# Optimization experiments

Hardware: AMD Instinct MI355X
Metric: run time of the kernel (lower is better)

Reference implementation:

```python
import jax, jax.numpy as jnp
import numpy as np

B, S, H, V, C = 32, 512, 256, 50000, 5
NUM_LAYERS, WINDOW = 2, 2


def setup_inputs() -> dict:
    key = jax.random.key(0)
    ks = jax.random.split(key, 24)
    std = 0.1  # matches nn.init.normal_(p, 0, 0.1)
    n = lambda k, shp: jax.random.normal(k, shp, dtype=jnp.float32) * std
    u = lambda k, shp: -0.05 + jax.random.uniform(k, shp, dtype=jnp.float32) * 0.1
    return {
        "input_sentences": jax.random.randint(ks[0], (B, S), 0, V),
        "sentences_length": jax.random.randint(ks[1], (B,), 1, S),
        "hh0": u(ks[2], (B, S, H)),
        "cs0": u(ks[3], (B, S, H)),
        "embed": n(ks[4], (V, H)),
        # stacked word-gate weights, gate order: i, l, r, f, s, output, u
        "W_lr": n(ks[5], (7, H, 2 * H)),
        "W_c": n(ks[6], (7, H, H)),
        "W_x": n(ks[7], (7, H, H)),
        "W_g": n(ks[8], (7, H, H)),
        "gate_bias": n(ks[9], (7, H)),
        # sentence-state gates
        "W_fg_g": n(ks[10], (H, H)),
        "W_fg_h": n(ks[11], (H, H)),
        "W_fgi_g": n(ks[12], (H, H)),
        "W_fgi_h": n(ks[13], (H, H)),
        "W_og_g": n(ks[14], (H, H)),
        "W_og_h": n(ks[15], (H, H)),
        "b_fg": n(ks[16], (H,)),
        "b_fgi": n(ks[17], (H,)),
        # output head
        "W1": n(ks[18], (H, 2 * H)),
        "b1": n(ks[19], (H,)),
        "Wout": n(ks[20], (C, H)),
        "bout": n(ks[21], (C,)),
    }


def _before_sum(x, window):
    # sum of right-shifted (zero-padded at front) copies, shifts 1..window
    out = jnp.zeros_like(x)
    for s in range(1, window + 1):
        out = out + jnp.pad(x[:, :-s], ((0, 0), (s, 0), (0, 0)))
    return out


def _after_sum(x, window):
    out = jnp.zeros_like(x)
    for s in range(1, window + 1):
        out = out + jnp.pad(x[:, s:], ((0, 0), (0, s), (0, 0)))
    return out


def _slstm_step(hh, cs, sv, scs, wv, W_lr, W_c, W_x, W_g, gate_bias,
                W_fg_g, W_fg_h, W_fgi_g, W_fgi_h, W_og_g, W_og_h, b_fg, b_fgi):
    avg_hh = hh.mean(axis=1)                                   # [B,H]
    f_hat_g = jax.nn.sigmoid(sv @ W_fg_g.T + avg_hh @ W_fg_h.T + b_fg)
    # NOTE: original code (faithfully) uses output_gate_bias here, not output_gate_g_bias
    og_g = jax.nn.sigmoid(sv @ W_og_g.T + avg_hh @ W_og_h.T + gate_bias[5])
    f_hat_g_i = jax.nn.sigmoid((sv @ W_fgi_g.T)[:, None] + hh @ W_fgi_h.T + b_fgi)
    scores = jax.nn.softmax(f_hat_g_i, axis=2)                 # over hidden dim
    new_scs = jax.nn.softmax(f_hat_g, axis=1) * scs + (scores * cs).sum(axis=1)
    new_sv = og_g * jnp.tanh(new_scs)

    hb = _before_sum(hh, WINDOW)
    ha = _after_sum(hh, WINDOW)
    cb = _before_sum(cs, WINDOW)
    ca = _after_sum(cs, WINDOW)
    ba = jnp.concatenate([hb, ha], axis=-1)                    # [B,S,2H]

    # all 7 gate pre-activations at once: [B,S,7,H]
    pre = (jnp.einsum('bsk,ghk->bsgh', ba, W_lr)
           + jnp.einsum('bsk,ghk->bsgh', hh, W_c)
           + jnp.einsum('bsk,ghk->bsgh', wv, W_x)
           + (jnp.einsum('bk,ghk->bgh', new_sv, W_g) + gate_bias)[:, None])

    g5 = jax.nn.sigmoid(pre[..., :5, :])                       # i,l,r,f,s
    b_, s_ = g5.shape[:2]
    # joint softmax over the concatenated 5*H gate vector (as in torch cat+softmax)
    g5 = jax.nn.softmax(g5.reshape(b_, s_, -1), axis=-1).reshape(b_, s_, 5, -1)
    i_t, l_t, r_t, f_t, s_t = (g5[..., k, :] for k in range(5))
    og = jax.nn.sigmoid(pre[..., 5, :])
    u_g = jnp.tanh(pre[..., 6, :])

    new_cs = l_t * cb + f_t * cs + r_t * ca + s_t * scs[:, None] + i_t * u_g
    new_hh = og * jnp.tanh(new_cs)
    return new_hh, new_cs, new_sv, new_scs


def reference(input_sentences, sentences_length, hh0, cs0, embed,
              W_lr, W_c, W_x, W_g, gate_bias,
              W_fg_g, W_fg_h, W_fgi_g, W_fgi_h, W_og_g, W_og_h, b_fg, b_fgi,
              W1, b1, Wout, bout):
    wv = embed[input_sentences]                                # [B,S,H]
    hh, cs = hh0, cs0
    sv, scs = hh0.mean(axis=1), cs0.mean(axis=1)
    for _ in range(NUM_LAYERS):
        hh, cs, sv, scs = _slstm_step(hh, cs, sv, scs, wv,
                                      W_lr, W_c, W_x, W_g, gate_bias,
                                      W_fg_g, W_fg_h, W_fgi_g, W_fgi_h,
                                      W_og_g, W_og_h, b_fg, b_fgi)
    avg_hh = hh.mean(axis=1)
    conc = jnp.concatenate([avg_hh, sv], axis=1) @ W1.T + b1
    fc = conc @ Wout.T + bout
    return jax.nn.log_softmax(fc, axis=1), sv
```

## Files before the change

kernel.cpp:

```cpp
#include <hip/hip_runtime.h>
#include <stdint.h>
#include <math.h>

#define B_   32
#define S_   512
#define H_   256
#define M_   (B_*S_)
#define KBIG 1024
#define NB   1792
#define C_   5

typedef __bf16 bf16;
typedef __bf16 bf16x8 __attribute__((ext_vector_type(8)));
typedef float  floatx4 __attribute__((ext_vector_type(4)));

__device__ __forceinline__ float sigm(float x){ return 1.f/(1.f+expf(-x)); }

__device__ __forceinline__ void gl16(const bf16* g, bf16* l){
    __builtin_amdgcn_global_load_lds(
        (const __attribute__((address_space(1))) unsigned int*)g,
        (__attribute__((address_space(3))) unsigned int*)l, 16, 0, 0);
}

__global__ void wcomb_k(const float* __restrict__ Wlr, const float* __restrict__ Wc,
                        const float* __restrict__ Wx, bf16* __restrict__ WT){
    int n = blockIdx.x;
    int g = n >> 8, h = n & 255;
    int k4 = threadIdx.x * 4;
    const float* src;
    if (k4 < 512)      src = Wlr + ((size_t)(g*256 + h))*512 + k4;
    else if (k4 < 768) src = Wc  + ((size_t)(g*256 + h))*256 + (k4 - 512);
    else               src = Wx  + ((size_t)(g*256 + h))*256 + (k4 - 768);
    float4 v = *(const float4*)src;
    bf16 o[4] = {(bf16)v.x,(bf16)v.y,(bf16)v.z,(bf16)v.w};
    *(uint2*)&WT[(size_t)n*KBIG + k4] = *(uint2*)o;
}

__global__ void cvtw_k(const float* __restrict__ a, bf16* __restrict__ o){
    int i4 = (blockIdx.x*256 + threadIdx.x)*4;
    float4 v = *(const float4*)(a + i4);
    bf16 t[4] = {(bf16)v.x,(bf16)v.y,(bf16)v.z,(bf16)v.w};
    *(uint2*)(o + i4) = *(uint2*)t;
}

__global__ void gather_k(const int* __restrict__ idx, const float* __restrict__ embed,
                         bf16* __restrict__ wv){
    int i4 = (blockIdx.x*256 + threadIdx.x)*4;
    int m = i4 >> 8, h = i4 & 255;
    float4 v = *(const float4*)(embed + (size_t)idx[m]*H_ + h);
    bf16 o[4] = {(bf16)v.x,(bf16)v.y,(bf16)v.z,(bf16)v.w};
    *(uint2*)(wv + (size_t)m*H_ + h) = *(uint2*)o;
}

__global__ void mean1_k(const float* __restrict__ x, float* __restrict__ part){
    int b = blockIdx.x, c = blockIdx.y, h = threadIdx.x;
    const float* p = x + ((size_t)b*S_ + c*32)*H_ + h;
    float s = 0.f;
    #pragma unroll 8
    for (int t=0;t<32;t++) s += p[(size_t)t*H_];
    part[((size_t)b*16 + c)*H_ + h] = s;
}
__global__ void mean2_k(const float* __restrict__ part, float* __restrict__ out){
    int b = blockIdx.x, h = threadIdx.x;
    float s = 0.f;
    #pragma unroll
    for (int c=0;c<16;c++) s += part[((size_t)b*16 + c)*H_ + h];
    out[b*H_ + h] = s * (1.f/512.f);
}

__global__ void buildx_k(const float* __restrict__ hh, const bf16* __restrict__ wv,
                         bf16* __restrict__ X){
    int m = blockIdx.x, h = threadIdx.x;
    int s = m & (S_-1);
    size_t base = (size_t)m*H_ + h;
    float hb = (s>=1    ? hh[base - H_] : 0.f) + (s>=2    ? hh[base - 2*H_] : 0.f);
    float ha = (s<=S_-2 ? hh[base + H_] : 0.f) + (s<=S_-3 ? hh[base + 2*H_] : 0.f);
    bf16* xr = X + (size_t)m*KBIG;
    xr[h]     = (bf16)hb;
    xr[256+h] = (bf16)ha;
    xr[512+h] = (bf16)hh[base];
    xr[768+h] = wv[base];
}

__global__ void mv5_k(const float* __restrict__ sv, const float* __restrict__ avg,
    const float* __restrict__ Wfg_g, const float* __restrict__ Wfg_h,
    const float* __restrict__ Wog_g, const float* __restrict__ Wog_h,
    const float* __restrict__ Wfgi_g, float* __restrict__ res){
    int j = blockIdx.x, b = blockIdx.y, h = threadIdx.x;
    const float* vec = (j==1 || j==3) ? avg + b*H_ : sv + b*H_;
    const float* W   = (j==0)?Wfg_g:(j==1)?Wfg_h:(j==2)?Wog_g:(j==3)?Wog_h:Wfgi_g;
    __shared__ float v[H_];
    v[h] = vec[h]; __syncthreads();
    const float* w = W + (size_t)h*H_;
    float d = 0.f;
    for (int k=0;k<H_;k++) d += v[k]*w[k];
    res[((size_t)b*5 + j)*H_ + h] = d;
}
__global__ void comb_k(const float* __restrict__ res, const float* __restrict__ b_fg,
                       const float* __restrict__ gbias, const float* __restrict__ b_fgi,
                       float* __restrict__ fhg, float* __restrict__ ogg,
                       float* __restrict__ svg){
    int b = blockIdx.x, h = threadIdx.x;
    const float* r = res + (size_t)b*5*H_;
    fhg[b*H_+h] = sigm(r[h] + r[H_+h] + b_fg[h]);
    ogg[b*H_+h] = sigm(r[2*H_+h] + r[3*H_+h] + gbias[5*H_+h]);
    svg[b*H_+h] = r[4*H_+h] + b_fgi[h];
}

template<int EPI>
__global__ __launch_bounds__(256)
void mgemm_k(const bf16* __restrict__ A, const bf16* __restrict__ BT,
             bf16* __restrict__ C, const float* __restrict__ gt,
             int Kdim, int lda, int ldb, int ldc){
    __shared__ alignas(16) bf16 lsA[128*32];
    __shared__ alignas(16) bf16 lsB[128*32];
    int tid  = threadIdx.x;
    int m0 = blockIdx.y * 128, n0 = blockIdx.x * 128;
    int wave = tid >> 6, lane = tid & 63;
    int wm = (wave & 1) * 64, wn = (wave >> 1) * 64;
    int lrow = lane & 15, quad = lane >> 4;

    floatx4 zero = {0.f,0.f,0.f,0.f};
    floatx4 acc[4][4];
    #pragma unroll
    for (int i=0;i<4;i++)
        #pragma unroll
        for (int j=0;j<4;j++) acc[i][j] = zero;

    int srow = tid >> 2;
    int scol = (tid & 3) * 8;
    const bf16* Abase = A  + (size_t)(m0 + srow)*lda + scol;
    const bf16* Bbase = BT + (size_t)(n0 + srow)*ldb + scol;
    bf16* dA0 = &lsA[srow*32 + scol];
    bf16* dA1 = &lsA[(64+srow)*32 + scol];
    bf16* dB0 = &lsB[srow*32 + scol];
    bf16* dB1 = &lsB[(64+srow)*32 + scol];

    for (int k0 = 0; k0 < Kdim; k0 += 32){
        __syncthreads();
        gl16(Abase + k0,                     dA0);
        gl16(Abase + (size_t)64*lda + k0,    dA1);
        gl16(Bbase + k0,                     dB0);
        gl16(Bbase + (size_t)64*ldb + k0,    dB1);
        __syncthreads();
        bf16x8 af[4], bfr[4];
        #pragma unroll
        for (int mi=0;mi<4;mi++) af[mi]  = *(const bf16x8*)&lsA[(wm+mi*16+lrow)*32 + quad*8];
        #pragma unroll
        for (int ni=0;ni<4;ni++) bfr[ni] = *(const bf16x8*)&lsB[(wn+ni*16+lrow)*32 + quad*8];
        #pragma unroll
        for (int mi=0;mi<4;mi++)
            #pragma unroll
            for (int ni=0;ni<4;ni++)
                acc[mi][ni] = __builtin_amdgcn_mfma_f32_16x16x32_bf16(af[mi], bfr[ni], acc[mi][ni], 0, 0, 0);
    }

    #pragma unroll
    for (int mi=0;mi<4;mi++)
        #pragma unroll
        for (int ni=0;ni<4;ni++){
            int row = m0 + wm + mi*16 + quad*4;
            int col = n0 + wn + ni*16 + lrow;
            #pragma unroll
            for (int r=0;r<4;r++){
                float v = acc[mi][ni][r];
                if (EPI) v += gt[(size_t)((row+r)>>9)*NB + col];
                C[(size_t)(row+r)*ldc + col] = (bf16)v;
            }
        }
}

__global__ void scorep_k(const bf16* __restrict__ fgih, const float* __restrict__ svg,
                         const float* __restrict__ cs, float* __restrict__ part){
    int chunk = blockIdx.x, b = blockIdx.y;
    int tid = threadIdx.x, wave = tid >> 6, lane = tid & 63;
    __shared__ float acc4[4][256];
    float sw[4], acc[4] = {0.f,0.f,0.f,0.f};
    #pragma unroll
    for (int j=0;j<4;j++) sw[j] = svg[b*H_ + lane + 64*j];
    for (int t=wave; t<16; t+=4){
        int m = b*S_ + chunk*16 + t;
        const bf16* fr = fgih + (size_t)m*H_;
        float e[4], loc = 0.f;
        #pragma unroll
        for (int j=0;j<4;j++){ e[j] = expf(sigm(sw[j] + (float)fr[lane+64*j])); loc += e[j]; }
        #pragma unroll
        for (int off=32; off; off>>=1) loc += __shfl_xor(loc, off, 64);
        float inv = 1.f/loc;
        const float* cr = cs + (size_t)m*H_;
        #pragma unroll
        for (int j=0;j<4;j++) acc[j] += e[j]*inv*cr[lane+64*j];
    }
    #pragma unroll
    for (int j=0;j<4;j++) acc4[wave][lane+64*j] = acc[j];
    __syncthreads();
    part[((size_t)b*32 + chunk)*H_ + tid] =
        acc4[0][tid] + acc4[1][tid] + acc4[2][tid] + acc4[3][tid];
}

__global__ void newscs_k(const float* __restrict__ part, const float* __restrict__ fhg,
                         const float* __restrict__ ogg, const float* __restrict__ scs_in,
                         float* __restrict__ scs_out, float* __restrict__ sv_out){
    int b = blockIdx.x, h = threadIdx.x;
    __shared__ float r[256];
    float dot = 0.f;
    #pragma unroll 8
    for (int c=0;c<32;c++) dot += part[((size_t)b*32+c)*H_ + h];
    float e = expf(fhg[b*H_+h]);
    r[h] = e; __syncthreads();
    for (int off=128; off; off>>=1){ if (h<off) r[h] += r[h+off]; __syncthreads(); }
    float ns = (e / r[0]) * scs_in[b*H_+h] + dot;
    scs_out[b*H_+h] = ns;
    sv_out[b*H_+h]  = ogg[b*H_+h] * tanhf(ns);
}

__global__ void gterm_k(const float* __restrict__ svn, const float* __restrict__ Wg,
                        const float* __restrict__ gbias, float* __restrict__ gt){
    int g = blockIdx.x, b = blockIdx.y, h = threadIdx.x;
    __shared__ float s[H_];
    s[h] = svn[b*H_+h]; __syncthreads();
    const float* w = Wg + ((size_t)g*H_ + h)*H_;
    float d = 0.f;
    for (int k=0;k<H_;k++) d += s[k]*w[k];
    gt[(size_t)b*NB + g*H_ + h] = d + gbias[g*H_+h];
}

__global__ void gates_k(const bf16* __restrict__ pre, const float* __restrict__ cs_in,
                        const float* __restrict__ scs_in,
                        float* __restrict__ hh_out, float* __restrict__ cs_out){
    int tid = threadIdx.x, wave = tid >> 6, lane = tid & 63;
    int m = blockIdx.x*4 + wave;
    int b = m >> 9, s = m & (S_-1);
    const bf16* row = pre + (size_t)m*NB;
    float ex[4][5], og[4], u[4];
    float loc = 0.f;
    #pragma unroll
    for (int j=0;j<4;j++){
        int h = lane + 64*j;
        #pragma unroll
        for (int g=0; g<5; ++g){
            float e = expf(sigm((float)row[g*H_ + h]));
            ex[j][g] = e; loc += e;
        }
        og[j] = sigm((float)row[5*H_ + h]);
        u[j]  = tanhf((float)row[6*H_ + h]);
    }
    #pragma unroll
    for (int off=32; off; off>>=1) loc += __shfl_xor(loc, off, 64);
    float inv = 1.f / loc;
    #pragma unroll
    for (int j=0;j<4;j++){
        int h = lane + 64*j;
        size_t i = (size_t)m*H_ + h;
        float cb = (s>=1    ? cs_in[i - H_] : 0.f) + (s>=2    ? cs_in[i - 2*H_] : 0.f);
        float ca = (s<=S_-2 ? cs_in[i + H_] : 0.f) + (s<=S_-3 ? cs_in[i + 2*H_] : 0.f);
        float nc = ex[j][1]*inv*cb + ex[j][3]*inv*cs_in[i] + ex[j][2]*inv*ca
                 + ex[j][4]*inv*scs_in[b*H_+h] + ex[j][0]*inv*u[j];
        cs_out[i] = nc;
        hh_out[i] = og[j] * tanhf(nc);
    }
}

__global__ void head_k(const float* __restrict__ avgh, const float* __restrict__ sv,
                       const float* __restrict__ W1, const float* __restrict__ b1,
                       const float* __restrict__ Wout, const float* __restrict__ bout,
                       float* __restrict__ out){
    int b = blockIdx.x, t = threadIdx.x;
    __shared__ float conc[H_];
    __shared__ float fc[8];
    const float* wr = W1 + (size_t)t*512;
    float d = b1[t];
    for (int k=0;k<H_;k++) d += avgh[b*H_+k]*wr[k];
    for (int k=0;k<H_;k++) d += sv[b*H_+k]*wr[256+k];
    conc[t] = d;
    __syncthreads();
    if (t < C_){
        const float* wo = Wout + (size_t)t*H_;
        float s = bout[t];
        for (int i=0;i<H_;i++) s += conc[i]*wo[i];
        fc[t] = s;
    }
    __syncthreads();
    if (t == 0){
        float mx = fc[0];
        for (int c=1;c<C_;c++) mx = fmaxf(mx, fc[c]);
        float se = 0.f;
        for (int c=0;c<C_;c++) se += expf(fc[c]-mx);
        float lse = mx + logf(se);
        for (int c=0;c<C_;c++) out[b*C_+c] = fc[c]-lse;
    }
    out[B_*C_ + b*H_ + t] = sv[b*H_+t];
}

extern "C" void kernel_launch(void* const* d_in, const int* in_sizes, int n_in,
                              void* d_out, int out_size, void* d_ws, size_t ws_size,
                              hipStream_t stream){
    const int*   idx    = (const int*)d_in[0];
    const float* hh0    = (const float*)d_in[2];
    const float* cs0    = (const float*)d_in[3];
    const float* embed  = (const float*)d_in[4];
    const float* Wlr    = (const float*)d_in[5];
    const float* Wc     = (const float*)d_in[6];
    const float* Wx     = (const float*)d_in[7];
    const float* Wg     = (const float*)d_in[8];
    const float* gbias  = (const float*)d_in[9];
    const float* Wfg_g  = (const float*)d_in[10];
    const float* Wfg_h  = (const float*)d_in[11];
    const float* Wfgi_g = (const float*)d_in[12];
    const float* Wfgi_h = (const float*)d_in[13];
    const float* Wog_g  = (const float*)d_in[14];
    const float* Wog_h  = (const float*)d_in[15];
    const float* b_fg   = (const float*)d_in[16];
    const float* b_fgi  = (const float*)d_in[17];
    const float* W1     = (const float*)d_in[18];
    const float* b1     = (const float*)d_in[19];
    const float* Wout   = (const float*)d_in[20];
    const float* bout   = (const float*)d_in[21];

    uint8_t* p = (uint8_t*)d_ws;
    auto alloc = [&](size_t bytes)->void*{ void* r=(void*)p; p += (bytes + 255) & ~(size_t)255; return r; };
    bf16*  WT    = (bf16*)alloc((size_t)NB*KBIG*2);
    bf16*  WfgiT = (bf16*)alloc((size_t)H_*H_*2);
    bf16*  X     = (bf16*)alloc((size_t)M_*KBIG*2);
    bf16*  wv    = (bf16*)alloc((size_t)M_*H_*2);
    bf16*  pre   = (bf16*)alloc((size_t)M_*NB*2);
    bf16*  fgih  = (bf16*)alloc((size_t)M_*H_*2);
    float* hhA = (float*)alloc((size_t)M_*H_*4);
    float* csA = (float*)alloc((size_t)M_*H_*4);
    float* hhB = (float*)alloc((size_t)M_*H_*4);
    float* csB = (float*)alloc((size_t)M_*H_*4);
    float* mpart= (float*)alloc((size_t)B_*16*H_*4);
    float* part = (float*)alloc((size_t)B_*32*H_*4);
    float* res5 = (float*)alloc((size_t)B_*5*H_*4);
    float* avgh = (float*)alloc(B_*H_*4);
    float* fhg  = (float*)alloc(B_*H_*4);
    float* ogg  = (float*)alloc(B_*H_*4);
    float* svg  = (float*)alloc(B_*H_*4);
    float* svP0 = (float*)alloc(B_*H_*4);
    float* svP1 = (float*)alloc(B_*H_*4);
    float* scP0 = (float*)alloc(B_*H_*4);
    float* scP1 = (float*)alloc(B_*H_*4);
    float* gt   = (float*)alloc((size_t)B_*NB*4);

    wcomb_k <<<NB,          256, 0, stream>>>(Wlr, Wc, Wx, WT);
    cvtw_k  <<<(H_*H_)/1024,256, 0, stream>>>(Wfgi_h, WfgiT);
    gather_k<<<(M_*H_)/1024,256, 0, stream>>>(idx, embed, wv);
    mean1_k <<<dim3(B_,16), 256, 0, stream>>>(hh0, mpart);
    mean2_k <<<B_,          256, 0, stream>>>(mpart, svP0);
    mean1_k <<<dim3(B_,16), 256, 0, stream>>>(cs0, mpart);
    mean2_k <<<B_,          256, 0, stream>>>(mpart, scP0);

    const float *hin = hh0, *cin = cs0;
    float *hout = hhA, *cout = csA;
    float *svin = svP0, *scin = scP0, *svout = svP1, *scout = scP1;

    for (int l=0; l<2; ++l){
        const float* avgp;
        if (l == 0){
            avgp = svin;
        } else {
            mean1_k<<<dim3(B_,16), 256, 0, stream>>>(hin, mpart);
            mean2_k<<<B_,          256, 0, stream>>>(mpart, avgh);
            avgp = avgh;
        }
        mv5_k   <<<dim3(5,B_), 256, 0, stream>>>(svin, avgp, Wfg_g, Wfg_h, Wog_g,
                                                 Wog_h, Wfgi_g, res5);
        comb_k  <<<B_, 256, 0, stream>>>(res5, b_fg, gbias, b_fgi, fhg, ogg, svg);
        buildx_k<<<M_, 256, 0, stream>>>(hin, wv, X);
        mgemm_k<0><<<dim3(2,128), 256, 0, stream>>>(X+512, WfgiT, fgih, nullptr,
                                                    H_, KBIG, H_, H_);
        scorep_k<<<dim3(32,B_), 256, 0, stream>>>(fgih, svg, cin, part);
        newscs_k<<<B_, 256, 0, stream>>>(part, fhg, ogg, scin, scout, svout);
        gterm_k <<<dim3(7,B_), 256, 0, stream>>>(svout, Wg, gbias, gt);
        mgemm_k<1><<<dim3(14,128), 256, 0, stream>>>(X, WT, pre, gt,
                                                     KBIG, KBIG, KBIG, NB);
        gates_k <<<M_/4, 256, 0, stream>>>(pre, cin, scin, hout, cout);
        hin = hout; cin = cout;
        hout = (l==0) ? hhB : hhA;
        cout = (l==0) ? csB : csA;
        float* q;
        q = svin; svin = svout; svout = q;
        q = scin; scin = scout; scout = q;
    }
    mean1_k<<<dim3(B_,16), 256, 0, stream>>>(hin, mpart);
    mean2_k<<<B_,          256, 0, stream>>>(mpart, avgh);
    head_k <<<B_, 256, 0, stream>>>(avgh, svin, W1, b1, Wout, bout, (float*)d_out);
}
```

Measured before the change: 571.8 us.

## Widen GEMM tiles to 128x256 and vectorize elementwise kernels with float4 loads

The bf16 MFMA GEMM now computes a 128x256 output tile per block, reusing each A fragment across two B sub-tiles. This halves the grid and the A-tile reloads. The buildx, scorep and gates kernels switch from strided scalar accesses to contiguous 4-wide vector loads and stores per lane, and buildx handles four rows per block. The wider tile doubles accumulator registers, which may reduce occupancy, and the smaller grids (128 and 896 blocks) may underfill the GPU.

```diff
diff --git a/kernel.cpp b/kernel.cpp
--- a/kernel.cpp
+++ b/kernel.cpp
@@ -70,16 +70,27 @@
 
 __global__ void buildx_k(const float* __restrict__ hh, const bf16* __restrict__ wv,
                          bf16* __restrict__ X){
-    int m = blockIdx.x, h = threadIdx.x;
+    int tid = threadIdx.x, wave = tid >> 6, lane = tid & 63;
+    int m = blockIdx.x*4 + wave;
     int s = m & (S_-1);
-    size_t base = (size_t)m*H_ + h;
-    float hb = (s>=1    ? hh[base - H_] : 0.f) + (s>=2    ? hh[base - 2*H_] : 0.f);
-    float ha = (s<=S_-2 ? hh[base + H_] : 0.f) + (s<=S_-3 ? hh[base + 2*H_] : 0.f);
+    int h0 = lane*4;
+    const float* hr = hh + (size_t)m*H_ + h0;
+    float hb[4] = {0,0,0,0}, ha[4] = {0,0,0,0};
+    if (s>=1){    float4 a = *(const float4*)(hr - H_);   hb[0]+=a.x; hb[1]+=a.y; hb[2]+=a.z; hb[3]+=a.w; }
+    if (s>=2){    float4 a = *(const float4*)(hr - 2*H_); hb[0]+=a.x; hb[1]+=a.y; hb[2]+=a.z; hb[3]+=a.w; }
+    if (s<=S_-2){ float4 a = *(const float4*)(hr + H_);   ha[0]+=a.x; ha[1]+=a.y; ha[2]+=a.z; ha[3]+=a.w; }
+    if (s<=S_-3){ float4 a = *(const float4*)(hr + 2*H_); ha[0]+=a.x; ha[1]+=a.y; ha[2]+=a.z; ha[3]+=a.w; }
+    float4 hc = *(const float4*)hr;
+    uint2 wvv = *(const uint2*)(wv + (size_t)m*H_ + h0);
     bf16* xr = X + (size_t)m*KBIG;
-    xr[h]     = (bf16)hb;
-    xr[256+h] = (bf16)ha;
-    xr[512+h] = (bf16)hh[base];
-    xr[768+h] = wv[base];
+    bf16 o[4];
+    o[0]=(bf16)hb[0]; o[1]=(bf16)hb[1]; o[2]=(bf16)hb[2]; o[3]=(bf16)hb[3];
+    *(uint2*)(xr + h0) = *(uint2*)o;
+    o[0]=(bf16)ha[0]; o[1]=(bf16)ha[1]; o[2]=(bf16)ha[2]; o[3]=(bf16)ha[3];
+    *(uint2*)(xr + 256 + h0) = *(uint2*)o;
+    o[0]=(bf16)hc.x;  o[1]=(bf16)hc.y;  o[2]=(bf16)hc.z;  o[3]=(bf16)hc.w;
+    *(uint2*)(xr + 512 + h0) = *(uint2*)o;
+    *(uint2*)(xr + 768 + h0) = wvv;
 }
 
 __global__ void mv5_k(const float* __restrict__ sv, const float* __restrict__ avg,
@@ -112,62 +123,76 @@
 void mgemm_k(const bf16* __restrict__ A, const bf16* __restrict__ BT,
              bf16* __restrict__ C, const float* __restrict__ gt,
              int Kdim, int lda, int ldb, int ldc){
-    __shared__ alignas(16) bf16 lsA[128*32];
-    __shared__ alignas(16) bf16 lsB[128*32];
+    __shared__ alignas(16) bf16 lsA [128*32];
+    __shared__ alignas(16) bf16 lsB0[128*32];
+    __shared__ alignas(16) bf16 lsB1[128*32];
     int tid  = threadIdx.x;
-    int m0 = blockIdx.y * 128, n0 = blockIdx.x * 128;
+    int m0 = blockIdx.y * 128, n0 = blockIdx.x * 256;
     int wave = tid >> 6, lane = tid & 63;
     int wm = (wave & 1) * 64, wn = (wave >> 1) * 64;
     int lrow = lane & 15, quad = lane >> 4;
 
     floatx4 zero = {0.f,0.f,0.f,0.f};
-    floatx4 acc[4][4];
-    #pragma unroll
-    for (int i=0;i<4;i++)
-        #pragma unroll
-        for (int j=0;j<4;j++) acc[i][j] = zero;
+    floatx4 acc[2][4][4];
+    #pragma unroll
+    for (int t=0;t<2;t++)
+        #pragma unroll
+        for (int i=0;i<4;i++)
+            #pragma unroll
+            for (int j=0;j<4;j++) acc[t][i][j] = zero;
 
     int srow = tid >> 2;
     int scol = (tid & 3) * 8;
-    const bf16* Abase = A  + (size_t)(m0 + srow)*lda + scol;
-    const bf16* Bbase = BT + (size_t)(n0 + srow)*ldb + scol;
-    bf16* dA0 = &lsA[srow*32 + scol];
-    bf16* dA1 = &lsA[(64+srow)*32 + scol];
-    bf16* dB0 = &lsB[srow*32 + scol];
-    bf16* dB1 = &lsB[(64+srow)*32 + scol];
+    const bf16* Abase  = A  + (size_t)(m0 + srow)*lda + scol;
+    const bf16* B0base = BT + (size_t)(n0 + srow)*ldb + scol;
+    const bf16* B1base = BT + (size_t)(n0 + 128 + srow)*ldb + scol;
+    bf16* dA0 = &lsA [srow*32 + scol];
+    bf16* dA1 = &lsA [(64+srow)*32 + scol];
+    bf16* dB00= &lsB0[srow*32 + scol];
+    bf16* dB01= &lsB0[(64+srow)*32 + scol];
+    bf16* dB10= &lsB1[srow*32 + scol];
+    bf16* dB11= &lsB1[(64+srow)*32 + scol];
 
     for (int k0 = 0; k0 < Kdim; k0 += 32){
         __syncthreads();
-        gl16(Abase + k0,                     dA0);
-        gl16(Abase + (size_t)64*lda + k0,    dA1);
-        gl16(Bbase + k0,                     dB0);
-        gl16(Bbase + (size_t)64*ldb + k0,    dB1);
+        gl16(Abase  + k0,                  dA0);
+        gl16(Abase  + (size_t)64*lda + k0, dA1);
+        gl16(B0base + k0,                  dB00);
+        gl16(B0base + (size_t)64*ldb + k0, dB01);
+        gl16(B1base + k0,                  dB10);
+        gl16(B1base + (size_t)64*ldb + k0, dB11);
         __syncthreads();
-        bf16x8 af[4], bfr[4];
-        #pragma unroll
-        for (int mi=0;mi<4;mi++) af[mi]  = *(const bf16x8*)&lsA[(wm+mi*16+lrow)*32 + quad*8];
-        #pragma unroll
-        for (int ni=0;ni<4;ni++) bfr[ni] = *(const bf16x8*)&lsB[(wn+ni*16+lrow)*32 + quad*8];
+        bf16x8 af[4], b0[4], b1[4];
+        #pragma unroll
+        for (int mi=0;mi<4;mi++) af[mi] = *(const bf16x8*)&lsA [(wm+mi*16+lrow)*32 + quad*8];
+        #pragma unroll
+        for (int ni=0;ni<4;ni++) b0[ni] = *(const bf16x8*)&lsB0[(wn+ni*16+lrow)*32 + quad*8];
+        #pragma unroll
+        for (int ni=0;ni<4;ni++) b1[ni] = *(const bf16x8*)&lsB1[(wn+ni*16+lrow)*32 + quad*8];
         #pragma unroll
         for (int mi=0;mi<4;mi++)
             #pragma unroll
-            for (int ni=0;ni<4;ni++)
-                acc[mi][ni] = __builtin_amdgcn_mfma_f32_16x16x32_bf16(af[mi], bfr[ni], acc[mi][ni], 0, 0, 0);
-    }
-
-    #pragma unroll
-    for (int mi=0;mi<4;mi++)
-        #pragma unroll
-        for (int ni=0;ni<4;ni++){
-            int row = m0 + wm + mi*16 + quad*4;
-            int col = n0 + wn + ni*16 + lrow;
+            for (int ni=0;ni<4;ni++){
+                acc[0][mi][ni] = __builtin_amdgcn_mfma_f32_16x16x32_bf16(af[mi], b0[ni], acc[0][mi][ni], 0, 0, 0);
+                acc[1][mi][ni] = __builtin_amdgcn_mfma_f32_16x16x32_bf16(af[mi], b1[ni], acc[1][mi][ni], 0, 0, 0);
+            }
+    }
+
+    #pragma unroll
+    for (int t=0;t<2;t++)
+        #pragma unroll
+        for (int mi=0;mi<4;mi++)
             #pragma unroll
-            for (int r=0;r<4;r++){
-                float v = acc[mi][ni][r];
-                if (EPI) v += gt[(size_t)((row+r)>>9)*NB + col];
-                C[(size_t)(row+r)*ldc + col] = (bf16)v;
+            for (int ni=0;ni<4;ni++){
+                int row = m0 + wm + mi*16 + quad*4;
+                int col = n0 + t*128 + wn + ni*16 + lrow;
+                #pragma unroll
+                for (int r=0;r<4;r++){
+                    float v = acc[t][mi][ni][r];
+                    if (EPI) v += gt[(size_t)((row+r)>>9)*NB + col];
+                    C[(size_t)(row+r)*ldc + col] = (bf16)v;
+                }
             }
-        }
 }
 
 __global__ void scorep_k(const bf16* __restrict__ fgih, const float* __restrict__ svg,
@@ -175,24 +200,24 @@
     int chunk = blockIdx.x, b = blockIdx.y;
     int tid = threadIdx.x, wave = tid >> 6, lane = tid & 63;
     __shared__ float acc4[4][256];
-    float sw[4], acc[4] = {0.f,0.f,0.f,0.f};
-    #pragma unroll
-    for (int j=0;j<4;j++) sw[j] = svg[b*H_ + lane + 64*j];
+    int h0 = lane*4;
+    float4 sw = *(const float4*)(svg + b*H_ + h0);
+    float swa[4] = {sw.x, sw.y, sw.z, sw.w};
+    float acc[4] = {0.f,0.f,0.f,0.f};
     for (int t=wave; t<16; t+=4){
         int m = b*S_ + chunk*16 + t;
-        const bf16* fr = fgih + (size_t)m*H_;
+        bf16 fv[4]; *(uint2*)fv = *(const uint2*)(fgih + (size_t)m*H_ + h0);
         float e[4], loc = 0.f;
         #pragma unroll
-        for (int j=0;j<4;j++){ e[j] = expf(sigm(sw[j] + (float)fr[lane+64*j])); loc += e[j]; }
+        for (int j=0;j<4;j++){ e[j] = expf(sigm(swa[j] + (float)fv[j])); loc += e[j]; }
         #pragma unroll
         for (int off=32; off; off>>=1) loc += __shfl_xor(loc, off, 64);
         float inv = 1.f/loc;
-        const float* cr = cs + (size_t)m*H_;
-        #pragma unroll
-        for (int j=0;j<4;j++) acc[j] += e[j]*inv*cr[lane+64*j];
-    }
-    #pragma unroll
-    for (int j=0;j<4;j++) acc4[wave][lane+64*j] = acc[j];
+        float4 cr = *(const float4*)(cs + (size_t)m*H_ + h0);
+        acc[0] += e[0]*inv*cr.x; acc[1] += e[1]*inv*cr.y;
+        acc[2] += e[2]*inv*cr.z; acc[3] += e[3]*inv*cr.w;
+    }
+    *(float4*)&acc4[wave][h0] = *(float4*)acc;
     __syncthreads();
     part[((size_t)b*32 + chunk)*H_ + tid] =
         acc4[0][tid] + acc4[1][tid] + acc4[2][tid] + acc4[3][tid];
@@ -231,34 +256,45 @@
     int tid = threadIdx.x, wave = tid >> 6, lane = tid & 63;
     int m = blockIdx.x*4 + wave;
     int b = m >> 9, s = m & (S_-1);
-    const bf16* row = pre + (size_t)m*NB;
-    float ex[4][5], og[4], u[4];
+    int h0 = lane*4;
+    const bf16* row = pre + (size_t)m*NB + h0;
+    float ex[5][4], og[4], u[4];
     float loc = 0.f;
     #pragma unroll
-    for (int j=0;j<4;j++){
-        int h = lane + 64*j;
-        #pragma unroll
-        for (int g=0; g<5; ++g){
-            float e = expf(sigm((float)row[g*H_ + h]));
-            ex[j][g] = e; loc += e;
-        }
-        og[j] = sigm((float)row[5*H_ + h]);
-        u[j]  = tanhf((float)row[6*H_ + h]);
-    }
+    for (int g=0; g<5; ++g){
+        bf16 v[4]; *(uint2*)v = *(const uint2*)(row + g*H_);
+        #pragma unroll
+        for (int j=0;j<4;j++){ float e = expf(sigm((float)v[j])); ex[g][j] = e; loc += e; }
+    }
+    { bf16 v[4]; *(uint2*)v = *(const uint2*)(row + 5*H_);
+      #pragma unroll
+      for (int j=0;j<4;j++) og[j] = sigm((float)v[j]); }
+    { bf16 v[4]; *(uint2*)v = *(const uint2*)(row + 6*H_);
+      #pragma unroll
+      for (int j=0;j<4;j++) u[j]  = tanhf((float)v[j]); }
     #pragma unroll
     for (int off=32; off; off>>=1) loc += __shfl_xor(loc, off, 64);
     float inv = 1.f / loc;
+    size_t i = (size_t)m*H_ + h0;
+    float4 cm = *(const float4*)(cs_in + i);
+    float cb[4] = {0,0,0,0}, ca[4] = {0,0,0,0};
+    if (s>=1){    float4 a = *(const float4*)(cs_in + i - H_);   cb[0]+=a.x; cb[1]+=a.y; cb[2]+=a.z; cb[3]+=a.w; }
+    if (s>=2){    float4 a = *(const float4*)(cs_in + i - 2*H_); cb[0]+=a.x; cb[1]+=a.y; cb[2]+=a.z; cb[3]+=a.w; }
+    if (s<=S_-2){ float4 a = *(const float4*)(cs_in + i + H_);   ca[0]+=a.x; ca[1]+=a.y; ca[2]+=a.z; ca[3]+=a.w; }
+    if (s<=S_-3){ float4 a = *(const float4*)(cs_in + i + 2*H_); ca[0]+=a.x; ca[1]+=a.y; ca[2]+=a.z; ca[3]+=a.w; }
+    float4 sc = *(const float4*)(scs_in + b*H_ + h0);
+    float scv[4] = {sc.x, sc.y, sc.z, sc.w};
+    float cmv[4] = {cm.x, cm.y, cm.z, cm.w};
+    float ncs[4], nhh[4];
     #pragma unroll
     for (int j=0;j<4;j++){
-        int h = lane + 64*j;
-        size_t i = (size_t)m*H_ + h;
-        float cb = (s>=1    ? cs_in[i - H_] : 0.f) + (s>=2    ? cs_in[i - 2*H_] : 0.f);
-        float ca = (s<=S_-2 ? cs_in[i + H_] : 0.f) + (s<=S_-3 ? cs_in[i + 2*H_] : 0.f);
-        float nc = ex[j][1]*inv*cb + ex[j][3]*inv*cs_in[i] + ex[j][2]*inv*ca
-                 + ex[j][4]*inv*scs_in[b*H_+h] + ex[j][0]*inv*u[j];
-        cs_out[i] = nc;
-        hh_out[i] = og[j] * tanhf(nc);
-    }
+        float nc = ex[1][j]*inv*cb[j] + ex[3][j]*inv*cmv[j] + ex[2][j]*inv*ca[j]
+                 + ex[4][j]*inv*scv[j] + ex[0][j]*inv*u[j];
+        ncs[j] = nc;
+        nhh[j] = og[j] * tanhf(nc);
+    }
+    *(float4*)(cs_out + i) = *(float4*)ncs;
+    *(float4*)(hh_out + i) = *(float4*)nhh;
 }
 
 __global__ void head_k(const float* __restrict__ avgh, const float* __restrict__ sv,
@@ -366,14 +402,14 @@
         mv5_k   <<<dim3(5,B_), 256, 0, stream>>>(svin, avgp, Wfg_g, Wfg_h, Wog_g,
                                                  Wog_h, Wfgi_g, res5);
         comb_k  <<<B_, 256, 0, stream>>>(res5, b_fg, gbias, b_fgi, fhg, ogg, svg);
-        buildx_k<<<M_, 256, 0, stream>>>(hin, wv, X);
-        mgemm_k<0><<<dim3(2,128), 256, 0, stream>>>(X+512, WfgiT, fgih, nullptr,
+        buildx_k<<<M_/4, 256, 0, stream>>>(hin, wv, X);
+        mgemm_k<0><<<dim3(1,128), 256, 0, stream>>>(X+512, WfgiT, fgih, nullptr,
                                                     H_, KBIG, H_, H_);
         scorep_k<<<dim3(32,B_), 256, 0, stream>>>(fgih, svg, cin, part);
         newscs_k<<<B_, 256, 0, stream>>>(part, fhg, ogg, scin, scout, svout);
         gterm_k <<<dim3(7,B_), 256, 0, stream>>>(svout, Wg, gbias, gt);
-        mgemm_k<1><<<dim3(14,128), 256, 0, stream>>>(X, WT, pre, gt,
-                                                     KBIG, KBIG, KBIG, NB);
+        mgemm_k<1><<<dim3(7,128), 256, 0, stream>>>(X, WT, pre, gt,
+                                                    KBIG, KBIG, KBIG, NB);
         gates_k <<<M_/4, 256, 0, stream>>>(pre, cin, scin, hout, cout);
         hin = hout; cin = cout;
         hout = (l==0) ? hhB : hhA;
```

Result: slower. 702.9 us (+22.9%).
